# Optimization experiments

Measured on AMD Instinct MI355X. Metric: run time of the kernel, lower is better.

## Reference

```python
import jax, jax.numpy as jnp
import numpy as np

B, H, S, D = 2, 16, 2048, 64  # depth = dmodel / num_heads
DMODEL = H * D


def setup_inputs() -> dict:
    key = jax.random.key(0)
    kq, kk, kv, kw = jax.random.split(key, 4)
    Q = jax.random.normal(kq, (B, H, S, D), dtype=jnp.float32)
    K = jax.random.normal(kk, (B, H, S, D), dtype=jnp.float32)
    V = jax.random.normal(kv, (B, H, S, D), dtype=jnp.float32)
    W = jax.random.normal(kw, (DMODEL, DMODEL), dtype=jnp.float32) * (1.0 / np.sqrt(DMODEL))
    b = jnp.zeros((DMODEL,), dtype=jnp.float32)
    return {"Q": Q, "K": K, "V": V, "W": W, "b": b}


def reference(Q, K, V, W, b):
    depth = Q.shape[-1]
    # scores: (B, H, S, S) -- full score matrix, matching the original math
    scores = jnp.einsum('bhqd,bhkd->bhqk', Q, K) / jnp.sqrt(jnp.float32(depth))
    attn = jax.nn.softmax(scores, axis=-1)
    vals = jnp.einsum('bhqk,bhkd->bhqd', attn, V)          # (B, H, S, D)
    vals = jnp.transpose(vals, (0, 2, 1, 3))               # (B, S, H, D)
    concat = vals.reshape(vals.shape[0], vals.shape[1], -1)  # (B, S, dmodel)
    return concat @ W + b
```

## Files before the change

kernel.cpp:

```cpp
#include <hip/hip_runtime.h>
#include <hip/hip_bf16.h>


typedef float  f32x16 __attribute__((ext_vector_type(16)));
typedef float  f32x4v __attribute__((ext_vector_type(4)));
typedef float  f32x2v __attribute__((ext_vector_type(2)));
typedef __bf16 bf16x8 __attribute__((ext_vector_type(8)));
typedef __bf16 bf16x4 __attribute__((ext_vector_type(4)));
typedef __bf16 bf16x2 __attribute__((ext_vector_type(2)));

static constexpr int Bn = 2, Hn = 16, Sn = 2048, Dn = 64, DM = 1024;
static constexpr size_t QKV_ELEMS = (size_t)Bn * Hn * Sn * Dn;

#define QSCALE 0.18033688011112042f

#if __has_builtin(__builtin_amdgcn_cvt_pk_bf16_f32)
static __device__ __forceinline__ unsigned pack2(float a, float b) {
  bf16x2 t = __builtin_amdgcn_cvt_pk_bf16_f32(a, b);
  union { bf16x2 v; unsigned u; } c; c.v = t; return c.u;
}
#else
static __device__ __forceinline__ unsigned pack2(float a, float b) {
  union { __bf16 h; unsigned short s; } ua, ub;
  ua.h = (__bf16)a; ub.h = (__bf16)b;
  return (unsigned)ua.s | ((unsigned)ub.s << 16);
}
#endif

static __device__ __forceinline__ void unzip8(const unsigned* wds, bf16x8* r0, bf16x8* r1) {
  union { unsigned u[4]; bf16x8 v; } a, b;
#pragma unroll
  for (int i = 0; i < 4; ++i) {
    unsigned lo = wds[2 * i], hi = wds[2 * i + 1];
    a.u[i] = (lo & 0xffffu) | (hi << 16);
    b.u[i] = (lo >> 16) | (hi & 0xffff0000u);
  }
  *r0 = a.v; *r1 = b.v;
}

__global__ __launch_bounds__(256) void convert_all(
    const float* __restrict__ q, const float* __restrict__ k,
    const float* __restrict__ v, const float* __restrict__ w,
    __bf16* __restrict__ qo, __bf16* __restrict__ ko,
    __bf16* __restrict__ vt, __bf16* __restrict__ wt) {
  __shared__ __bf16 T[64][74];
  const int bid = blockIdx.x, t = threadIdx.x;

  if (bid < 4096) {
    const int z = bid >> 11;
    const int bx = bid & 2047;
    const float* src = z ? k : q;
    __bf16* dst      = z ? ko : qo;
    const float scale = z ? 1.0f : QSCALE;
    size_t i = ((size_t)bx * 256 + t) * 8;
    f32x4v a = *(const f32x4v*)(src + i);
    f32x4v b = *(const f32x4v*)(src + i + 4);
    bf16x8 o;
#pragma unroll
    for (int j = 0; j < 4; ++j) { o[j] = (__bf16)(a[j] * scale); o[4 + j] = (__bf16)(b[j] * scale); }
    *(bf16x8*)(dst + i) = o;
    return;
  }

  const float* s0;
  __bf16* dst0;
  size_t dst_stride;
  {
    const int r = t >> 2, c0 = (t & 3) * 16;
    if (bid < 5120) {
      const int idx = bid - 4096;
      const int kv0 = (idx & 31) * 64, bh = idx >> 5;
      s0 = v + ((size_t)bh * Sn + kv0 + r) * Dn + c0;
      dst0 = vt + (size_t)bh * Dn * Sn + kv0;
      dst_stride = Sn;
    } else {
      const int idx = bid - 5120;
      const int nt = (idx & 15) * 64, kt = (idx >> 4) * 64;
      s0 = w + (size_t)(kt + r) * DM + nt + c0;
      dst0 = wt + (size_t)nt * DM + kt;
      dst_stride = DM;
    }
    union { bf16x8 v8; unsigned u[4]; } o0, o1;
#pragma unroll
    for (int i = 0; i < 2; ++i) {
      f32x4v f = *(const f32x4v*)(s0 + i * 4);
#pragma unroll
      for (int j = 0; j < 4; ++j) o0.v8[i * 4 + j] = (__bf16)f[j];
    }
#pragma unroll
    for (int i = 0; i < 2; ++i) {
      f32x4v f = *(const f32x4v*)(s0 + 8 + i * 4);
#pragma unroll
      for (int j = 0; j < 4; ++j) o1.v8[i * 4 + j] = (__bf16)f[j];
    }
#pragma unroll
    for (int j = 0; j < 4; ++j) {
      *(unsigned*)&T[r][c0 + 2 * j]     = o0.u[j];
      *(unsigned*)&T[r][c0 + 8 + 2 * j] = o1.u[j];
    }
  }
  __syncthreads();
  const int rp = t >> 3, k0 = (t & 7) * 8;
  unsigned wds[8];
#pragma unroll
  for (int i = 0; i < 8; ++i) wds[i] = *(const unsigned*)&T[k0 + i][2 * rp];
  bf16x8 r0, r1; unzip8(wds, &r0, &r1);
  __bf16* d0 = dst0 + (size_t)(2 * rp) * dst_stride + k0;
  *(bf16x8*)d0 = r0;
  *(bf16x8*)(d0 + dst_stride) = r1;
}

__global__ __launch_bounds__(256, 3) void attn(
    const __bf16* __restrict__ Qb, const __bf16* __restrict__ Kb,
    const __bf16* __restrict__ Vtg, __bf16* __restrict__ Cc) {
  const int tid = threadIdx.x;
  const int wave = tid >> 6, lane = tid & 63;
  const int ln = lane & 31, g = lane >> 5;
  const int qg = wave >> 1, kh = wave & 1;
  const int qb = blockIdx.x, h = blockIdx.y, bz = blockIdx.z;

  __shared__ char pool[2 * 64 * 72 * 2 + 2 * 64 * 76 * 2];
  __bf16 (*Ks)[64][72] = (__bf16(*)[64][72])pool;
  __bf16 (*Vs)[64][76] = (__bf16(*)[64][76])(pool + 2 * 64 * 72 * 2);

  const size_t hoff = (size_t)(bz * Hn + h) * Sn * Dn;
  const __bf16* Qp = Qb + hoff + (size_t)(qb * 128 + qg * 64) * Dn;
  const __bf16* Kp = Kb + hoff;
  const __bf16* Vp = Vtg + hoff;

  bf16x8 qf[2][4];
#pragma unroll
  for (int qt = 0; qt < 2; ++qt)
#pragma unroll
    for (int ks = 0; ks < 4; ++ks)
      qf[qt][ks] = *(const bf16x8*)(Qp + (size_t)(qt * 32 + ln) * Dn + ks * 16 + g * 8);

  const int sr = tid >> 2, sc = (tid & 3) * 16;
  const __bf16* kbase = Kp + (size_t)sr * Dn + sc;
  const __bf16* vbase = Vp + (size_t)sr * Sn + sc;

  bf16x8 k0r = *(const bf16x8*)kbase, k1r = *(const bf16x8*)(kbase + 8);
  bf16x8 v0r = *(const bf16x8*)vbase, v1r = *(const bf16x8*)(vbase + 8);
  {
    *(bf16x8*)&Ks[0][sr][sc]     = k0r;
    *(bf16x8*)&Ks[0][sr][sc + 8] = k1r;
    union { bf16x8 v; bf16x4 h[2]; } u0, u1; u0.v = v0r; u1.v = v1r;
    *(bf16x4*)&Vs[0][sr][sc]      = u0.h[0];
    *(bf16x4*)&Vs[0][sr][sc + 4]  = u0.h[1];
    *(bf16x4*)&Vs[0][sr][sc + 8]  = u1.h[0];
    *(bf16x4*)&Vs[0][sr][sc + 12] = u1.h[1];
  }
  k0r = *(const bf16x8*)(kbase + (size_t)64 * Dn);
  k1r = *(const bf16x8*)(kbase + (size_t)64 * Dn + 8);
  v0r = *(const bf16x8*)(vbase + 64);
  v1r = *(const bf16x8*)(vbase + 64 + 8);
  __syncthreads();

  f32x16 O[2][2] = {{{}, {}}, {{}, {}}};
  float Lown[2] = {0.0f, 0.0f};
  constexpr int NT = Sn / 64;

  for (int kt = 0; kt < NT; ++kt) {
    const int buf = kt & 1;

    bf16x8 kf[4];
#pragma unroll
    for (int ks = 0; ks < 4; ++ks)
      kf[ks] = *(const bf16x8*)&Ks[buf][kh * 32 + ln][ks * 16 + g * 8];

    unsigned w[2][8];
#pragma unroll
    for (int qt = 0; qt < 2; ++qt) {
      f32x16 s = {};
#pragma unroll
      for (int ks = 0; ks < 4; ++ks)
        s = __builtin_amdgcn_mfma_f32_32x32x16_bf16(kf[ks], qf[qt][ks], s, 0, 0, 0);
      float p[16];
#pragma unroll
      for (int r = 0; r < 16; ++r) p[r] = __builtin_amdgcn_exp2f(s[r]);
      f32x2v s2 = {0.0f, 0.0f};
#pragma unroll
      for (int tt = 0; tt < 8; ++tt) { f32x2v t2 = {p[2 * tt], p[2 * tt + 1]}; s2 += t2; }
      Lown[qt] += s2[0] + s2[1];
#pragma unroll
      for (int tt = 0; tt < 8; ++tt) w[qt][tt] = pack2(p[2 * tt], p[2 * tt + 1]);
    }

    if (kt + 1 < NT) {
      const int nb = buf ^ 1;
      *(bf16x8*)&Ks[nb][sr][sc]     = k0r;
      *(bf16x8*)&Ks[nb][sr][sc + 8] = k1r;
      union { bf16x8 v; bf16x4 h[2]; } u0, u1; u0.v = v0r; u1.v = v1r;
      *(bf16x4*)&Vs[nb][sr][sc]      = u0.h[0];
      *(bf16x4*)&Vs[nb][sr][sc + 4]  = u0.h[1];
      *(bf16x4*)&Vs[nb][sr][sc + 8]  = u1.h[0];
      *(bf16x4*)&Vs[nb][sr][sc + 12] = u1.h[1];
      if (kt + 2 < NT) {
        const __bf16* kp = kbase + (size_t)(kt + 2) * 64 * Dn;
        k0r = *(const bf16x8*)kp; k1r = *(const bf16x8*)(kp + 8);
        const __bf16* vp = vbase + (kt + 2) * 64;
        v0r = *(const bf16x8*)vp; v1r = *(const bf16x8*)(vp + 8);
      }
    }

#pragma unroll
    for (int s4 = 0; s4 < 2; ++s4) {
      const int cb = kh * 32 + s4 * 16 + g * 4;
      union { bf16x4 h[2]; bf16x8 v; } vf0, vf1;
      vf0.h[0] = *(const bf16x4*)&Vs[buf][ln][cb];
      vf0.h[1] = *(const bf16x4*)&Vs[buf][ln][cb + 8];
      vf1.h[0] = *(const bf16x4*)&Vs[buf][32 + ln][cb];
      vf1.h[1] = *(const bf16x4*)&Vs[buf][32 + ln][cb + 8];
#pragma unroll
      for (int qt = 0; qt < 2; ++qt) {
        union { unsigned u[4]; bf16x8 v; } pu;
        pu.u[0] = w[qt][s4 * 4 + 0];
        pu.u[1] = w[qt][s4 * 4 + 1];
        pu.u[2] = w[qt][s4 * 4 + 2];
        pu.u[3] = w[qt][s4 * 4 + 3];
        O[qt][0] = __builtin_amdgcn_mfma_f32_32x32x16_bf16(vf0.v, pu.v, O[qt][0], 0, 0, 0);
        O[qt][1] = __builtin_amdgcn_mfma_f32_32x32x16_bf16(vf1.v, pu.v, O[qt][1], 0, 0, 0);
      }
    }
    __syncthreads();
  }

  float Lred[2];
#pragma unroll
  for (int qt = 0; qt < 2; ++qt) Lred[qt] = Lown[qt] + __shfl_xor(Lown[qt], 32);

  float* Ex = (float*)pool;
  const int slot = (qg * 64 + lane) * 68;
  if (kh == 1) {
#pragma unroll
    for (int qt = 0; qt < 2; ++qt)
#pragma unroll
      for (int dh = 0; dh < 2; ++dh)
#pragma unroll
        for (int i = 0; i < 4; ++i) {
          f32x4v t = {O[qt][dh][4 * i], O[qt][dh][4 * i + 1],
                      O[qt][dh][4 * i + 2], O[qt][dh][4 * i + 3]};
          *(f32x4v*)&Ex[slot + qt * 32 + dh * 16 + 4 * i] = t;
        }
    Ex[slot + 64] = Lred[0];
    Ex[slot + 65] = Lred[1];
  }
  __syncthreads();
  float inv[2] = {0.0f, 0.0f};
  if (kh == 0) {
#pragma unroll
    for (int qt = 0; qt < 2; ++qt)
#pragma unroll
      for (int dh = 0; dh < 2; ++dh)
#pragma unroll
        for (int i = 0; i < 4; ++i) {
          f32x4v t = *(const f32x4v*)&Ex[slot + qt * 32 + dh * 16 + 4 * i];
#pragma unroll
          for (int c = 0; c < 4; ++c) O[qt][dh][4 * i + c] += t[c];
        }
    inv[0] = 1.0f / (Lred[0] + Ex[slot + 64]);
    inv[1] = 1.0f / (Lred[1] + Ex[slot + 65]);
  }
  __syncthreads();
  __bf16* T = (__bf16*)pool;
  if (kh == 0) {
#pragma unroll
    for (int qt = 0; qt < 2; ++qt)
#pragma unroll
      for (int dh = 0; dh < 2; ++dh)
#pragma unroll
        for (int a = 0; a < 4; ++a) {
          bf16x4 t4;
#pragma unroll
          for (int c = 0; c < 4; ++c) t4[c] = (__bf16)(O[qt][dh][4 * a + c] * inv[qt]);
          *(bf16x4*)&T[(qg * 64 + qt * 32 + ln) * 72 + dh * 32 + 8 * a + 4 * g] = t4;
        }
  }
  __syncthreads();
  const int q0 = qb * 128;
#pragma unroll
  for (int i = 0; i < 4; ++i) {
    const int rq = i * 32 + (tid >> 3);
    const int c8 = (tid & 7) * 8;
    bf16x8 o = *(const bf16x8*)&T[rq * 72 + c8];
    size_t base = (((size_t)bz * Sn + q0 + rq) * Hn + h) * Dn + c8;
    *(bf16x8*)&Cc[base] = o;
  }
}

__global__ __launch_bounds__(512, 2) void proj(
    const __bf16* __restrict__ A, const __bf16* __restrict__ Wt,
    const float* __restrict__ bias, float* __restrict__ out) {
  const int tid = threadIdx.x, wave = tid >> 6, lane = tid & 63;
  const int ln = lane & 31, g = lane >> 5;
  const int mq = wave >> 1, nh = wave & 1;
  const int bm = blockIdx.x, bn = blockIdx.y;
  __shared__ __bf16 As[2][128][72];
  __shared__ __bf16 Bs[2][64][72];
  const int ar = tid >> 2, ac = (tid & 3) * 16;
  const int rb = tid >> 3, cb = (tid & 7) * 8;
  f32x16 acc = {};
  const __bf16* Ap = A + (size_t)(bm * 128) * DM;
  const __bf16* Wp = Wt + (size_t)(bn * 64) * DM;

  bf16x8 a0, a1, b0;
  {
    const __bf16* ap = Ap + (size_t)ar * DM + ac;
    a0 = *(const bf16x8*)ap; a1 = *(const bf16x8*)(ap + 8);
    b0 = *(const bf16x8*)(Wp + (size_t)rb * DM + cb);
  }
  *(bf16x8*)&As[0][ar][ac]     = a0;
  *(bf16x8*)&As[0][ar][ac + 8] = a1;
  *(bf16x8*)&Bs[0][rb][cb]     = b0;
  {
    const __bf16* ap = Ap + (size_t)ar * DM + 64 + ac;
    a0 = *(const bf16x8*)ap; a1 = *(const bf16x8*)(ap + 8);
    b0 = *(const bf16x8*)(Wp + (size_t)rb * DM + 64 + cb);
  }
  __syncthreads();

  constexpr int KT = DM / 64;
  for (int kt = 0; kt < KT; ++kt) {
    const int buf = kt & 1;
#pragma unroll
    for (int ks = 0; ks < 4; ++ks) {
      bf16x8 af = *(const bf16x8*)&As[buf][mq * 32 + ln][ks * 16 + g * 8];
      bf16x8 wf = *(const bf16x8*)&Bs[buf][nh * 32 + ln][ks * 16 + g * 8];
      acc = __builtin_amdgcn_mfma_f32_32x32x16_bf16(af, wf, acc, 0, 0, 0);
    }
    if (kt + 1 < KT) {
      const int nb = buf ^ 1;
      *(bf16x8*)&As[nb][ar][ac]     = a0;
      *(bf16x8*)&As[nb][ar][ac + 8] = a1;
      *(bf16x8*)&Bs[nb][rb][cb]     = b0;
      if (kt + 2 < KT) {
        const __bf16* ap = Ap + (size_t)ar * DM + (kt + 2) * 64 + ac;
        a0 = *(const bf16x8*)ap; a1 = *(const bf16x8*)(ap + 8);
        b0 = *(const bf16x8*)(Wp + (size_t)rb * DM + (kt + 2) * 64 + cb);
      }
    }
    __syncthreads();
  }
  const float bv = bias[bn * 64 + nh * 32 + ln];
#pragma unroll
  for (int r = 0; r < 16; ++r) {
    int row = bm * 128 + mq * 32 + (r & 3) + 8 * (r >> 2) + 4 * g;
    out[(size_t)row * DM + bn * 64 + nh * 32 + ln] = acc[r] + bv;
  }
}

extern "C" void kernel_launch(void* const* d_in, const int* in_sizes, int n_in,
                              void* d_out, int out_size, void* d_ws, size_t ws_size,
                              hipStream_t stream) {
  const float* Q = (const float*)d_in[0];
  const float* K = (const float*)d_in[1];
  const float* V = (const float*)d_in[2];
  const float* W = (const float*)d_in[3];
  const float* b = (const float*)d_in[4];
  float* out = (float*)d_out;

  __bf16* ws  = (__bf16*)d_ws;
  __bf16* Qb  = ws;
  __bf16* Kb  = Qb + QKV_ELEMS;
  __bf16* Vtg = Kb + QKV_ELEMS;
  __bf16* Cc  = Vtg + QKV_ELEMS;
  __bf16* Wt  = Cc + QKV_ELEMS;

  convert_all<<<dim3(5376, 1, 1), 256, 0, stream>>>(Q, K, V, W, Qb, Kb, Vtg, Wt);
  attn<<<dim3(Sn / 128, Hn, Bn), 256, 0, stream>>>(Qb, Kb, Vtg, Cc);
  proj<<<dim3(Bn * Sn / 128, DM / 64, 1), 512, 0, stream>>>(Cc, Wt, b, out);
}
```

Measured before the change: 165.9 us.

## Halve attention query tile to 64 rows and raise occupancy target

The attention kernel now processes 64 query rows per block instead of 128, so each wave holds one 32-row query tile. The grid doubles to 1024 blocks, register pressure drops, and launch bounds ask for 4 blocks per CU. The V shared tile padding changes from 76 to 72 so stores can use 8-wide vectors. The cost is that each K/V tile loaded from global into shared memory is reused by half as many queries, doubling total K/V traffic and the per-tile sync overhead.

```diff
diff --git a/kernel.cpp b/kernel.cpp
--- a/kernel.cpp
+++ b/kernel.cpp
@@ -110,7 +110,7 @@
   *(bf16x8*)(d0 + dst_stride) = r1;
 }
 
-__global__ __launch_bounds__(256, 3) void attn(
+__global__ __launch_bounds__(256, 4) void attn(
     const __bf16* __restrict__ Qb, const __bf16* __restrict__ Kb,
     const __bf16* __restrict__ Vtg, __bf16* __restrict__ Cc) {
   const int tid = threadIdx.x;
@@ -119,21 +119,19 @@
   const int qg = wave >> 1, kh = wave & 1;
   const int qb = blockIdx.x, h = blockIdx.y, bz = blockIdx.z;
 
-  __shared__ char pool[2 * 64 * 72 * 2 + 2 * 64 * 76 * 2];
-  __bf16 (*Ks)[64][72] = (__bf16(*)[64][72])pool;
-  __bf16 (*Vs)[64][76] = (__bf16(*)[64][76])(pool + 2 * 64 * 72 * 2);
+  __shared__ __bf16 smem[2][2][64][72];
+  __bf16 (*Ks)[64][72] = smem[0];
+  __bf16 (*Vs)[64][72] = smem[1];
 
   const size_t hoff = (size_t)(bz * Hn + h) * Sn * Dn;
-  const __bf16* Qp = Qb + hoff + (size_t)(qb * 128 + qg * 64) * Dn;
+  const __bf16* Qp = Qb + hoff + (size_t)(qb * 64 + qg * 32) * Dn;
   const __bf16* Kp = Kb + hoff;
   const __bf16* Vp = Vtg + hoff;
 
-  bf16x8 qf[2][4];
-#pragma unroll
-  for (int qt = 0; qt < 2; ++qt)
-#pragma unroll
-    for (int ks = 0; ks < 4; ++ks)
-      qf[qt][ks] = *(const bf16x8*)(Qp + (size_t)(qt * 32 + ln) * Dn + ks * 16 + g * 8);
+  bf16x8 qf[4];
+#pragma unroll
+  for (int ks = 0; ks < 4; ++ks)
+    qf[ks] = *(const bf16x8*)(Qp + (size_t)ln * Dn + ks * 16 + g * 8);
 
   const int sr = tid >> 2, sc = (tid & 3) * 16;
   const __bf16* kbase = Kp + (size_t)sr * Dn + sc;
@@ -141,23 +139,18 @@
 
   bf16x8 k0r = *(const bf16x8*)kbase, k1r = *(const bf16x8*)(kbase + 8);
   bf16x8 v0r = *(const bf16x8*)vbase, v1r = *(const bf16x8*)(vbase + 8);
-  {
-    *(bf16x8*)&Ks[0][sr][sc]     = k0r;
-    *(bf16x8*)&Ks[0][sr][sc + 8] = k1r;
-    union { bf16x8 v; bf16x4 h[2]; } u0, u1; u0.v = v0r; u1.v = v1r;
-    *(bf16x4*)&Vs[0][sr][sc]      = u0.h[0];
-    *(bf16x4*)&Vs[0][sr][sc + 4]  = u0.h[1];
-    *(bf16x4*)&Vs[0][sr][sc + 8]  = u1.h[0];
-    *(bf16x4*)&Vs[0][sr][sc + 12] = u1.h[1];
-  }
+  *(bf16x8*)&Ks[0][sr][sc]     = k0r;
+  *(bf16x8*)&Ks[0][sr][sc + 8] = k1r;
+  *(bf16x8*)&Vs[0][sr][sc]     = v0r;
+  *(bf16x8*)&Vs[0][sr][sc + 8] = v1r;
   k0r = *(const bf16x8*)(kbase + (size_t)64 * Dn);
   k1r = *(const bf16x8*)(kbase + (size_t)64 * Dn + 8);
   v0r = *(const bf16x8*)(vbase + 64);
   v1r = *(const bf16x8*)(vbase + 64 + 8);
   __syncthreads();
 
-  f32x16 O[2][2] = {{{}, {}}, {{}, {}}};
-  float Lown[2] = {0.0f, 0.0f};
+  f32x16 O0 = {}, O1 = {};
+  float Lown = 0.0f;
   constexpr int NT = Sn / 64;
 
   for (int kt = 0; kt < NT; ++kt) {
@@ -168,33 +161,27 @@
     for (int ks = 0; ks < 4; ++ks)
       kf[ks] = *(const bf16x8*)&Ks[buf][kh * 32 + ln][ks * 16 + g * 8];
 
-    unsigned w[2][8];
-#pragma unroll
-    for (int qt = 0; qt < 2; ++qt) {
-      f32x16 s = {};
-#pragma unroll
-      for (int ks = 0; ks < 4; ++ks)
-        s = __builtin_amdgcn_mfma_f32_32x32x16_bf16(kf[ks], qf[qt][ks], s, 0, 0, 0);
-      float p[16];
-#pragma unroll
-      for (int r = 0; r < 16; ++r) p[r] = __builtin_amdgcn_exp2f(s[r]);
-      f32x2v s2 = {0.0f, 0.0f};
-#pragma unroll
-      for (int tt = 0; tt < 8; ++tt) { f32x2v t2 = {p[2 * tt], p[2 * tt + 1]}; s2 += t2; }
-      Lown[qt] += s2[0] + s2[1];
-#pragma unroll
-      for (int tt = 0; tt < 8; ++tt) w[qt][tt] = pack2(p[2 * tt], p[2 * tt + 1]);
-    }
+    f32x16 s = {};
+#pragma unroll
+    for (int ks = 0; ks < 4; ++ks)
+      s = __builtin_amdgcn_mfma_f32_32x32x16_bf16(kf[ks], qf[ks], s, 0, 0, 0);
+    float p[16];
+#pragma unroll
+    for (int r = 0; r < 16; ++r) p[r] = __builtin_amdgcn_exp2f(s[r]);
+    f32x2v s2 = {0.0f, 0.0f};
+#pragma unroll
+    for (int tt = 0; tt < 8; ++tt) { f32x2v t2 = {p[2 * tt], p[2 * tt + 1]}; s2 += t2; }
+    Lown += s2[0] + s2[1];
+    unsigned w[8];
+#pragma unroll
+    for (int tt = 0; tt < 8; ++tt) w[tt] = pack2(p[2 * tt], p[2 * tt + 1]);
 
     if (kt + 1 < NT) {
       const int nb = buf ^ 1;
       *(bf16x8*)&Ks[nb][sr][sc]     = k0r;
       *(bf16x8*)&Ks[nb][sr][sc + 8] = k1r;
-      union { bf16x8 v; bf16x4 h[2]; } u0, u1; u0.v = v0r; u1.v = v1r;
-      *(bf16x4*)&Vs[nb][sr][sc]      = u0.h[0];
-      *(bf16x4*)&Vs[nb][sr][sc + 4]  = u0.h[1];
-      *(bf16x4*)&Vs[nb][sr][sc + 8]  = u1.h[0];
-      *(bf16x4*)&Vs[nb][sr][sc + 12] = u1.h[1];
+      *(bf16x8*)&Vs[nb][sr][sc]     = v0r;
+      *(bf16x8*)&Vs[nb][sr][sc + 8] = v1r;
       if (kt + 2 < NT) {
         const __bf16* kp = kbase + (size_t)(kt + 2) * 64 * Dn;
         k0r = *(const bf16x8*)kp; k1r = *(const bf16x8*)(kp + 8);
@@ -211,75 +198,69 @@
       vf0.h[1] = *(const bf16x4*)&Vs[buf][ln][cb + 8];
       vf1.h[0] = *(const bf16x4*)&Vs[buf][32 + ln][cb];
       vf1.h[1] = *(const bf16x4*)&Vs[buf][32 + ln][cb + 8];
-#pragma unroll
-      for (int qt = 0; qt < 2; ++qt) {
-        union { unsigned u[4]; bf16x8 v; } pu;
-        pu.u[0] = w[qt][s4 * 4 + 0];
-        pu.u[1] = w[qt][s4 * 4 + 1];
-        pu.u[2] = w[qt][s4 * 4 + 2];
-        pu.u[3] = w[qt][s4 * 4 + 3];
-        O[qt][0] = __builtin_amdgcn_mfma_f32_32x32x16_bf16(vf0.v, pu.v, O[qt][0], 0, 0, 0);
-        O[qt][1] = __builtin_amdgcn_mfma_f32_32x32x16_bf16(vf1.v, pu.v, O[qt][1], 0, 0, 0);
+      union { unsigned u[4]; bf16x8 v; } pu;
+      pu.u[0] = w[s4 * 4 + 0];
+      pu.u[1] = w[s4 * 4 + 1];
+      pu.u[2] = w[s4 * 4 + 2];
+      pu.u[3] = w[s4 * 4 + 3];
+      O0 = __builtin_amdgcn_mfma_f32_32x32x16_bf16(vf0.v, pu.v, O0, 0, 0, 0);
+      O1 = __builtin_amdgcn_mfma_f32_32x32x16_bf16(vf1.v, pu.v, O1, 0, 0, 0);
+    }
+    __syncthreads();
+  }
+
+  const float Lred = Lown + __shfl_xor(Lown, 32);
+  float* Ex = (float*)smem;
+  const int slot = (qg * 64 + lane) * 36;
+  if (kh == 1) {
+#pragma unroll
+    for (int i = 0; i < 4; ++i) {
+      f32x4v t = {O0[4 * i], O0[4 * i + 1], O0[4 * i + 2], O0[4 * i + 3]};
+      *(f32x4v*)&Ex[slot + 4 * i] = t;
+    }
+#pragma unroll
+    for (int i = 0; i < 4; ++i) {
+      f32x4v t = {O1[4 * i], O1[4 * i + 1], O1[4 * i + 2], O1[4 * i + 3]};
+      *(f32x4v*)&Ex[slot + 16 + 4 * i] = t;
+    }
+    Ex[slot + 32] = Lred;
+  }
+  __syncthreads();
+  float inv = 0.0f;
+  if (kh == 0) {
+#pragma unroll
+    for (int i = 0; i < 4; ++i) {
+      f32x4v t = *(const f32x4v*)&Ex[slot + 4 * i];
+#pragma unroll
+      for (int c = 0; c < 4; ++c) O0[4 * i + c] += t[c];
+    }
+#pragma unroll
+    for (int i = 0; i < 4; ++i) {
+      f32x4v t = *(const f32x4v*)&Ex[slot + 16 + 4 * i];
+#pragma unroll
+      for (int c = 0; c < 4; ++c) O1[4 * i + c] += t[c];
+    }
+    inv = 1.0f / (Lred + Ex[slot + 32]);
+  }
+  __syncthreads();
+  __bf16* T = (__bf16*)smem;
+  if (kh == 0) {
+#pragma unroll
+    for (int dh = 0; dh < 2; ++dh) {
+#pragma unroll
+      for (int a = 0; a < 4; ++a) {
+        const f32x16 O = dh ? O1 : O0;
+        bf16x4 t4;
+#pragma unroll
+        for (int c = 0; c < 4; ++c) t4[c] = (__bf16)(O[4 * a + c] * inv);
+        *(bf16x4*)&T[(qg * 32 + ln) * 72 + dh * 32 + 8 * a + 4 * g] = t4;
       }
     }
-    __syncthreads();
-  }
-
-  float Lred[2];
-#pragma unroll
-  for (int qt = 0; qt < 2; ++qt) Lred[qt] = Lown[qt] + __shfl_xor(Lown[qt], 32);
-
-  float* Ex = (float*)pool;
-  const int slot = (qg * 64 + lane) * 68;
-  if (kh == 1) {
-#pragma unroll
-    for (int qt = 0; qt < 2; ++qt)
-#pragma unroll
-      for (int dh = 0; dh < 2; ++dh)
-#pragma unroll
-        for (int i = 0; i < 4; ++i) {
-          f32x4v t = {O[qt][dh][4 * i], O[qt][dh][4 * i + 1],
-                      O[qt][dh][4 * i + 2], O[qt][dh][4 * i + 3]};
-          *(f32x4v*)&Ex[slot + qt * 32 + dh * 16 + 4 * i] = t;
-        }
-    Ex[slot + 64] = Lred[0];
-    Ex[slot + 65] = Lred[1];
-  }
-  __syncthreads();
-  float inv[2] = {0.0f, 0.0f};
-  if (kh == 0) {
-#pragma unroll
-    for (int qt = 0; qt < 2; ++qt)
-#pragma unroll
-      for (int dh = 0; dh < 2; ++dh)
-#pragma unroll
-        for (int i = 0; i < 4; ++i) {
-          f32x4v t = *(const f32x4v*)&Ex[slot + qt * 32 + dh * 16 + 4 * i];
-#pragma unroll
-          for (int c = 0; c < 4; ++c) O[qt][dh][4 * i + c] += t[c];
-        }
-    inv[0] = 1.0f / (Lred[0] + Ex[slot + 64]);
-    inv[1] = 1.0f / (Lred[1] + Ex[slot + 65]);
-  }
-  __syncthreads();
-  __bf16* T = (__bf16*)pool;
-  if (kh == 0) {
-#pragma unroll
-    for (int qt = 0; qt < 2; ++qt)
-#pragma unroll
-      for (int dh = 0; dh < 2; ++dh)
-#pragma unroll
-        for (int a = 0; a < 4; ++a) {
-          bf16x4 t4;
-#pragma unroll
-          for (int c = 0; c < 4; ++c) t4[c] = (__bf16)(O[qt][dh][4 * a + c] * inv[qt]);
-          *(bf16x4*)&T[(qg * 64 + qt * 32 + ln) * 72 + dh * 32 + 8 * a + 4 * g] = t4;
-        }
-  }
-  __syncthreads();
-  const int q0 = qb * 128;
-#pragma unroll
-  for (int i = 0; i < 4; ++i) {
+  }
+  __syncthreads();
+  const int q0 = qb * 64;
+#pragma unroll
+  for (int i = 0; i < 2; ++i) {
     const int rq = i * 32 + (tid >> 3);
     const int c8 = (tid & 7) * 8;
     bf16x8 o = *(const bf16x8*)&T[rq * 72 + c8];
@@ -367,6 +348,6 @@
   __bf16* Wt  = Cc + QKV_ELEMS;
 
   convert_all<<<dim3(5376, 1, 1), 256, 0, stream>>>(Q, K, V, W, Qb, Kb, Vtg, Wt);
-  attn<<<dim3(Sn / 128, Hn, Bn), 256, 0, stream>>>(Qb, Kb, Vtg, Cc);
+  attn<<<dim3(Sn / 64, Hn, Bn), 256, 0, stream>>>(Qb, Kb, Vtg, Cc);
   proj<<<dim3(Bn * Sn / 128, DM / 64, 1), 512, 0, stream>>>(Cc, Wt, b, out);
 }
```

New measurement: 164.1 us. About the same (-1.1%).
